# Performance work log

Measured on AMD Instinct MI355X. Metric: run time of the kernel, lower is better.

Reference implementation:

```python
import jax, jax.numpy as jnp
import numpy as np

B, L, D = 8, 2048, 64

def setup_inputs() -> dict:
    key = jax.random.key(0)
    kq, kk, kv, kqm, kkm = jax.random.split(key, 5)
    return {
        "query": jax.random.normal(kq, (B, L, D), dtype=jnp.float32),
        "key": jax.random.normal(kk, (B, L, D), dtype=jnp.float32),
        "value": jax.random.normal(kv, (B, L, D), dtype=jnp.float32),
        "q_mask": jax.random.randint(kqm, (B, L), 0, 2, dtype=jnp.int32),
        "k_mask": jax.random.randint(kkm, (B, L), 0, 2, dtype=jnp.int32),
    }

def reference(query, key, value, q_mask, k_mask):
    # scale defaults to D_q; divide scores by sqrt(D_q)
    D_q = query.shape[-1]
    qm = q_mask.astype(jnp.float32)  # [B, L_q]
    km = k_mask.astype(jnp.float32)  # [B, L_k]
    # outer-product mask: [B, L_q, L_k]
    mask = qm[:, :, None] * km[:, None, :]
    scores = jnp.einsum("bqd,bkd->bqk", query, key) / jnp.sqrt(jnp.float32(D_q))
    # masked_fill(-inf).exp(): masked positions become exactly 0
    A = jnp.where(mask == 0, 0.0, jnp.exp(scores))  # [B, L_q, L_k]
    # sum clamped to min 1.0 (NOT a standard softmax normalization)
    A_sum = jnp.maximum(A.sum(axis=-1, keepdims=True), 1.0)
    attn = A / A_sum
    return jnp.einsum("bqk,bkd->bqd", attn, value)
```

## Files before the change

### kernel.cpp

```cpp
#include <hip/hip_runtime.h>
#include <hip/hip_bf16.h>
#include <stdint.h>

#define BB 8
#define LL 2048
#define DD 64

typedef short bf16x8 __attribute__((ext_vector_type(8)));
typedef float f32x4 __attribute__((ext_vector_type(4)));
typedef unsigned short ushort_t;
typedef __attribute__((address_space(1))) const unsigned int gas_u32;
typedef __attribute__((address_space(3))) unsigned int las_u32;

__device__ __forceinline__ unsigned pk2(float lo, float hi) {
    union { __hip_bfloat162 h; unsigned u; } c;
    c.h = __float22bfloat162_rn(make_float2(lo, hi));
    return c.u;
}
__device__ __forceinline__ float4 ld4(const float* __restrict__ p) {
    return *reinterpret_cast<const float4*>(p);
}
__device__ __forceinline__ bf16x8 cvt8f(float4 a, float4 b) {
    union { bf16x8 v; unsigned u[4]; } r;
    r.u[0] = pk2(a.x, a.y); r.u[1] = pk2(a.z, a.w);
    r.u[2] = pk2(b.x, b.y); r.u[3] = pk2(b.z, b.w);
    return r.v;
}
__device__ __forceinline__ void glds16(const void* g, void* lds_base_uniform) {
    __builtin_amdgcn_global_load_lds((gas_u32*)g, (las_u32*)lds_base_uniform, 16, 0, 0);
}
__device__ __forceinline__ unsigned f2bf_u(float f) {
    union { float f; unsigned u; } v; v.f = f;
    return (v.u + 0x8000u) >> 16;
}
__device__ __forceinline__ bf16x8 cvt8(const float* __restrict__ p) {
    float4 a = ld4(p), b = ld4(p + 4);
    union { bf16x8 v; unsigned u[4]; } r;
    r.u[0] = f2bf_u(a.x) | (f2bf_u(a.y) << 16);
    r.u[1] = f2bf_u(a.z) | (f2bf_u(a.w) << 16);
    r.u[2] = f2bf_u(b.x) | (f2bf_u(b.y) << 16);
    r.u[3] = f2bf_u(b.z) | (f2bf_u(b.w) << 16);
    return r.v;
}

__global__ __launch_bounds__(256) void prep(const float* __restrict__ K,
                                            const float* __restrict__ V,
                                            ushort_t* __restrict__ Kb,
                                            ushort_t* __restrict__ VT) {
    __shared__ float t[64][65];
    if (blockIdx.x < 512) {
        size_t i = ((size_t)blockIdx.x * 256 + threadIdx.x) * 8;
        float4 a = ld4(K + i), b = ld4(K + i + 4);
        uint4 o = { pk2(a.x, a.y), pk2(a.z, a.w), pk2(b.x, b.y), pk2(b.z, b.w) };
        *reinterpret_cast<uint4*>(Kb + i) = o;
        return;
    }
    const int bx = blockIdx.x - 512;
    const int b  = bx >> 5;
    const int kt = (bx & 31) << 6;
    {
        const int r  = threadIdx.x >> 2;
        const int cq = (threadIdx.x & 3) << 4;
        const float* src = V + ((size_t)(b * LL + kt + r)) * DD + cq;
        #pragma unroll
        for (int i = 0; i < 4; ++i) {
            float4 v = ld4(src + 4 * i);
            t[r][cq + 4 * i + 0] = v.x; t[r][cq + 4 * i + 1] = v.y;
            t[r][cq + 4 * i + 2] = v.z; t[r][cq + 4 * i + 3] = v.w;
        }
    }
    __syncthreads();
    {
        const int d  = threadIdx.x >> 2;
        const int kq = (threadIdx.x & 3) << 4;
        ushort_t* dst = VT + ((size_t)(b * DD + d)) * LL + kt + kq;
        #pragma unroll
        for (int u = 0; u < 2; ++u) {
            uint4 o;
            o.x = pk2(t[kq + 8 * u + 0][d], t[kq + 8 * u + 1][d]);
            o.y = pk2(t[kq + 8 * u + 2][d], t[kq + 8 * u + 3][d]);
            o.z = pk2(t[kq + 8 * u + 4][d], t[kq + 8 * u + 5][d]);
            o.w = pk2(t[kq + 8 * u + 6][d], t[kq + 8 * u + 7][d]);
            *reinterpret_cast<uint4*>(dst + 8 * u) = o;
        }
    }
}

__global__ __launch_bounds__(512, 4) void attn8(
    const float* __restrict__ Q,
    const ushort_t* __restrict__ Kbf,
    const ushort_t* __restrict__ VTb,
    const int* __restrict__ kmask,
    float* __restrict__ Opart)
{
    const int tid  = threadIdx.x;
    const int wave = tid >> 6;
    const int lane = tid & 63;
    const int ln   = lane & 15;
    const int quad = lane >> 4;

    const int bx    = blockIdx.x;
    const int ksp   = bx & 3;
    const int qt    = (bx >> 2) & 15;
    const int b     = bx >> 6;
    const int q0    = qt * 128;
    const int kbase = ksp * 512;

    __shared__ char  lds[3][16384];
    __shared__ float kmf[512];

    const char* Kg = (const char*)Kbf + (size_t)b * LL * DD * 2;
    const char* Vg = (const char*)VTb + (size_t)b * DD * LL * 2;
    const int gr = tid >> 3;
    const int gc = (tid & 7) ^ (gr & 7);

    #define STAGE(buf, k0)                                                     \
        do {                                                                   \
            glds16(Kg + (size_t)(kbase + (k0) + gr) * 128 + gc * 16,           \
                   &lds[buf][wave * 1024]);                                    \
            glds16(Vg + (size_t)gr * (LL * 2) + (kbase + (k0)) * 2 + gc * 16,  \
                   &lds[buf][8192 + wave * 1024]);                             \
        } while (0)

    const float* qp = Q + ((size_t)(b * LL + q0 + 16 * wave + ln)) * DD + quad * 8;
    float4 qa = ld4(qp), qb = ld4(qp + 4), qc = ld4(qp + 32), qd = ld4(qp + 36);
    int4 km4 = {0, 0, 0, 0};
    if (tid < 128)
        km4 = *reinterpret_cast<const int4*>(kmask + b * LL + kbase + tid * 4);

    STAGE(0, 0);
    STAGE(1, 64);

    bf16x8 qf[2];
    qf[0] = cvt8f(qa, qb);
    qf[1] = cvt8f(qc, qd);
    if (tid < 128) {
        float4 f = { km4.x ? 1.f : 0.f, km4.y ? 1.f : 0.f,
                     km4.z ? 1.f : 0.f, km4.w ? 1.f : 0.f };
        *reinterpret_cast<float4*>(kmf + tid * 4) = f;
    }
    asm volatile("s_waitcnt lgkmcnt(0)" ::: "memory");

    f32x4 Oacc[4] = {{0,0,0,0},{0,0,0,0},{0,0,0,0},{0,0,0,0}};
    float dsum = 0.f;
    const float EC = 0.125f * 1.44269504f;

    auto tile = [&](int cb_, int it_) {
        const char* LK = lds[cb_];
        const char* LV = lds[cb_] + 8192;

        bf16x8 kf[4][2];
        #pragma unroll
        for (int tt = 0; tt < 4; ++tt) {
            const int r = 16 * tt + ln;
            #pragma unroll
            for (int dh = 0; dh < 2; ++dh) {
                const int c = (dh * 4 + quad) ^ (ln & 7);
                kf[tt][dh] = *reinterpret_cast<const bf16x8*>(LK + r * 128 + c * 16);
            }
        }
        bf16x8 vf[2][4];
        #pragma unroll
        for (int kh = 0; kh < 2; ++kh) {
            const int c = (kh * 4 + quad) ^ (ln & 7);
            #pragma unroll
            for (int db = 0; db < 4; ++db) {
                const int d = db * 16 + ln;
                vf[kh][db] = *reinterpret_cast<const bf16x8*>(LV + d * 128 + c * 16);
            }
        }

        unsigned w[4][2];
        #pragma unroll
        for (int tt = 0; tt < 4; ++tt) {
            f32x4 acc = (f32x4){0.f, 0.f, 0.f, 0.f};
            __builtin_amdgcn_s_setprio(1);
            acc = __builtin_amdgcn_mfma_f32_16x16x32_bf16(kf[tt][0], qf[0], acc, 0, 0, 0);
            acc = __builtin_amdgcn_mfma_f32_16x16x32_bf16(kf[tt][1], qf[1], acc, 0, 0, 0);
            __builtin_amdgcn_s_setprio(0);
            float4 mu = *reinterpret_cast<const float4*>(
                kmf + it_ * 64 + 16 * tt + 4 * quad);
            float e0 = exp2f(acc[0] * EC) * mu.x;
            float e1 = exp2f(acc[1] * EC) * mu.y;
            float e2 = exp2f(acc[2] * EC) * mu.z;
            float e3 = exp2f(acc[3] * EC) * mu.w;
            dsum += (e0 + e1) + (e2 + e3);
            w[tt][0] = pk2(e0, e1);
            w[tt][1] = pk2(e2, e3);
        }
        #pragma unroll
        for (int g = 0; g < 2; ++g) {
            union { bf16x8 v; unsigned u[4]; } pf;
            #pragma unroll
            for (int r = 0; r < 2; ++r) {
                auto t32 = __builtin_amdgcn_permlane32_swap(
                    w[2 * g][r], w[2 * g + 1][r], false, false);
                auto t16 = __builtin_amdgcn_permlane16_swap(
                    t32[0], t32[1], false, false);
                pf.u[r]     = t16[0];
                pf.u[r + 2] = t16[1];
            }
            __builtin_amdgcn_s_setprio(1);
            #pragma unroll
            for (int db = 0; db < 4; ++db)
                Oacc[db] = __builtin_amdgcn_mfma_f32_16x16x32_bf16(
                    pf.v, vf[g][db], Oacc[db], 0, 0, 0);
            __builtin_amdgcn_s_setprio(0);
        }
    };

    int cb = 0;
    for (int it = 0; it < 7; ++it) {
        asm volatile("s_waitcnt vmcnt(2)" ::: "memory");
        __builtin_amdgcn_s_barrier();
        asm volatile("" ::: "memory");
        if (it < 6) {
            int sb = cb + 2; if (sb >= 3) sb -= 3;
            STAGE(sb, (it + 2) * 64);
        }
        tile(cb, it);
        cb = (cb == 2) ? 0 : cb + 1;
    }
    asm volatile("s_waitcnt vmcnt(0)" ::: "memory");
    __builtin_amdgcn_s_barrier();
    asm volatile("" ::: "memory");
    tile(cb, 7);
    #undef STAGE

    {
        float v = dsum;
        v += __shfl_xor(v, 16);
        v += __shfl_xor(v, 32);
        dsum = v;
    }

    float* pb = Opart + (size_t)bx * 8320;
    #pragma unroll
    for (int db = 0; db < 4; ++db)
        #pragma unroll
        for (int r = 0; r < 4; ++r)
            pb[(16 * wave + quad * 4 + r) * 64 + db * 16 + ln] = Oacc[db][r];
    if (quad == 0) pb[8192 + 16 * wave + ln] = dsum;
}

__global__ __launch_bounds__(256) void reduce_norm(
    const float* __restrict__ Opart,
    const int* __restrict__ qmask,
    float* __restrict__ Out)
{
    const int rb   = blockIdx.x;
    const int half = rb & 1;
    const int qt   = (rb >> 1) & 15;
    const int b    = rb >> 5;
    const int t    = threadIdx.x;
    const int q    = half * 64 + (t >> 2);
    const int d0   = (t & 3) * 16;

    const float* p0 = Opart + (size_t)((b * 16 + qt) * 4 + 0) * 8320;
    const float* p1 = p0 + 8320;
    const float* p2 = p1 + 8320;
    const float* p3 = p2 + 8320;

    float dn = p0[8192 + q] + p1[8192 + q] + p2[8192 + q] + p3[8192 + q];
    float sc = qmask[b * LL + qt * 128 + q] ? (1.0f / fmaxf(dn, 1.0f)) : 0.0f;

    const int off = q * 64 + d0;
    float* op = Out + ((size_t)(b * LL + qt * 128 + q)) * DD + d0;
    #pragma unroll
    for (int i = 0; i < 4; ++i) {
        f32x4 v = *reinterpret_cast<const f32x4*>(p0 + off + 4 * i)
                + *reinterpret_cast<const f32x4*>(p1 + off + 4 * i)
                + *reinterpret_cast<const f32x4*>(p2 + off + 4 * i)
                + *reinterpret_cast<const f32x4*>(p3 + off + 4 * i);
        *reinterpret_cast<f32x4*>(op + 4 * i) = v * sc;
    }
}

__global__ __launch_bounds__(256, 4) void attn_mfma(
    const float* __restrict__ Q, const float* __restrict__ K,
    const float* __restrict__ V, const int* __restrict__ qmask,
    const int* __restrict__ kmask, float* __restrict__ Out)
{
    const int tid  = threadIdx.x;
    const int wave = tid >> 6;
    const int lane = tid & 63;
    const int n    = lane & 15;
    const int quad = lane >> 4;
    const int bx = blockIdx.x;
    const int b  = bx >> 7;
    const int q0 = (bx & 127) << 4;
    __shared__ float Pl[4][576];
    __shared__ float Opart2[4][16][68];
    __shared__ float Denp[4][16];
    const float* Qp = Q + ((size_t)(b * LL + q0 + n)) * DD + quad * 8;
    bf16x8 qf0 = cvt8(Qp);
    bf16x8 qf1 = cvt8(Qp + 32);
    const float* Kb = K + ((size_t)(b * LL) + n) * DD + quad * 8;
    const float* Vb = V + ((size_t)(b * LL) + quad * 8) * DD + n;
    const int* kmb = kmask + b * LL;
    f32x4 Oacc[4] = {{0,0,0,0},{0,0,0,0},{0,0,0,0},{0,0,0,0}};
    float den[4]  = {0.f, 0.f, 0.f, 0.f};
    float*       pw = &Pl[wave][144 * (n >> 3) + 36 * quad + (n & 7)];
    const float* pr = &Pl[wave][9 * lane];
    const int kbeg = wave * (LL / 4);
    const int kend = kbeg + (LL / 4);
    for (int k0 = kbeg; k0 < kend; k0 += 32) {
        const float* krow = Kb + (size_t)k0 * DD;
        bf16x8 kA0 = cvt8(krow);
        bf16x8 kA1 = cvt8(krow + 32);
        bf16x8 kB0 = cvt8(krow + 16 * DD);
        bf16x8 kB1 = cvt8(krow + 16 * DD + 32);
        f32x4 z = {0.f, 0.f, 0.f, 0.f};
        f32x4 S0 = __builtin_amdgcn_mfma_f32_16x16x32_bf16(qf0, kA0, z, 0, 0, 0);
        S0 = __builtin_amdgcn_mfma_f32_16x16x32_bf16(qf1, kA1, S0, 0, 0, 0);
        f32x4 S1 = __builtin_amdgcn_mfma_f32_16x16x32_bf16(qf0, kB0, z, 0, 0, 0);
        S1 = __builtin_amdgcn_mfma_f32_16x16x32_bf16(qf1, kB1, S1, 0, 0, 0);
        float km0 = (float)kmb[k0 + n];
        float km1 = (float)kmb[k0 + 16 + n];
        #pragma unroll
        for (int r = 0; r < 4; ++r) {
            float e0 = __expf(S0[r] * 0.125f) * km0;
            float e1 = __expf(S1[r] * 0.125f) * km1;
            den[r] += e0 + e1;
            pw[9 * r]       = e0;
            pw[288 + 9 * r] = e1;
        }
        __builtin_amdgcn_wave_barrier();
        float pv[8];
        #pragma unroll
        for (int j = 0; j < 8; ++j) pv[j] = pr[j];
        __builtin_amdgcn_wave_barrier();
        union { bf16x8 v; unsigned u[4]; } pf;
        #pragma unroll
        for (int j = 0; j < 4; ++j)
            pf.u[j] = f2bf_u(pv[2 * j]) | (f2bf_u(pv[2 * j + 1]) << 16);
        const float* vrow = Vb + (size_t)k0 * DD;
        #pragma unroll
        for (int db = 0; db < 4; ++db) {
            union { bf16x8 v; unsigned u[4]; } vfr;
            #pragma unroll
            for (int jj = 0; jj < 4; ++jj) {
                unsigned lo  = f2bf_u(vrow[(2 * jj) * DD + db * 16]);
                unsigned hi2 = f2bf_u(vrow[(2 * jj + 1) * DD + db * 16]);
                vfr.u[jj] = lo | (hi2 << 16);
            }
            Oacc[db] = __builtin_amdgcn_mfma_f32_16x16x32_bf16(pf.v, vfr.v, Oacc[db], 0, 0, 0);
        }
    }
    #pragma unroll
    for (int r = 0; r < 4; ++r) {
        float v = den[r];
        v += __shfl_xor(v, 1); v += __shfl_xor(v, 2);
        v += __shfl_xor(v, 4); v += __shfl_xor(v, 8);
        den[r] = v;
    }
    #pragma unroll
    for (int db = 0; db < 4; ++db)
        #pragma unroll
        for (int r = 0; r < 4; ++r)
            Opart2[wave][quad * 4 + r][db * 16 + n] = Oacc[db][r];
    if (n == 0) {
        #pragma unroll
        for (int r = 0; r < 4; ++r) Denp[wave][quad * 4 + r] = den[r];
    }
    __syncthreads();
    const int q  = tid >> 4;
    const int d0 = (tid & 15) * 4;
    f32x4 sum = *reinterpret_cast<const f32x4*>(&Opart2[0][q][d0]);
    sum += *reinterpret_cast<const f32x4*>(&Opart2[1][q][d0]);
    sum += *reinterpret_cast<const f32x4*>(&Opart2[2][q][d0]);
    sum += *reinterpret_cast<const f32x4*>(&Opart2[3][q][d0]);
    float dn  = Denp[0][q] + Denp[1][q] + Denp[2][q] + Denp[3][q];
    float inv = 1.0f / fmaxf(dn, 1.0f);
    float s   = qmask[b * LL + q0 + q] ? inv : 0.0f;
    f32x4 o   = sum * s;
    float* op = Out + ((size_t)(b * LL + q0 + q)) * DD + d0;
    *reinterpret_cast<f32x4*>(op) = o;
}

extern "C" void kernel_launch(void* const* d_in, const int* in_sizes, int n_in,
                              void* d_out, int out_size, void* d_ws, size_t ws_size,
                              hipStream_t stream) {
    (void)in_sizes; (void)n_in; (void)out_size;
    const float* Q  = (const float*)d_in[0];
    const float* K  = (const float*)d_in[1];
    const float* V  = (const float*)d_in[2];
    const int* qm   = (const int*)d_in[3];
    const int* km   = (const int*)d_in[4];
    float* Out      = (float*)d_out;

    const size_t elems   = (size_t)BB * LL * DD;
    const size_t part_off = 4u * 1024 * 1024;
    const size_t ws_need  = part_off + (size_t)512 * 8320 * sizeof(float);
    if (ws_size >= ws_need && d_ws != nullptr) {
        ushort_t* Kbf = (ushort_t*)d_ws;
        ushort_t* VTb = Kbf + elems;
        float* Opart  = (float*)((char*)d_ws + part_off);
        prep       <<<dim3(768), dim3(256), 0, stream>>>(K, V, Kbf, VTb);
        attn8      <<<dim3(512), dim3(512), 0, stream>>>(Q, Kbf, VTb, km, Opart);
        reduce_norm<<<dim3(256), dim3(256), 0, stream>>>(Opart, qm, Out);
    } else {
        attn_mfma<<<dim3(BB * (LL / 16)), dim3(256), 0, stream>>>(Q, K, V, qm, km, Out);
    }
}
```

Measured before the change: 100.3 us.

## Fuse prep, attention and reduction into one cooperative kernel with grid syncs

Replaces the three-kernel sequence (K/V bf16 conversion and transpose, split-K attention, partial reduction and normalization) with a single cooperative launch that separates the phases with grid-wide barriers. The aim is to remove two kernel launch gaps and the tail idle time between dependent kernels. The prep and reduce phases are remapped onto 512 blocks of 512 threads, and the prep phase reuses the attention LDS buffer. In exchange, grid sync adds its own cost, and it requires all 512 blocks to be co-resident. If the cooperative launch fails, the code falls back to the old three-kernel path.

```diff
diff --git a/kernel.cpp b/kernel.cpp
--- a/kernel.cpp
+++ b/kernel.cpp
@@ -1,10 +1,13 @@
 #include <hip/hip_runtime.h>
+#include <hip/hip_cooperative_groups.h>
 #include <hip/hip_bf16.h>
 #include <stdint.h>
 
 #define BB 8
 #define LL 2048
 #define DD 64
+
+namespace cg = cooperative_groups;
 
 typedef short bf16x8 __attribute__((ext_vector_type(8)));
 typedef float f32x4 __attribute__((ext_vector_type(4)));
@@ -43,55 +46,14 @@
     return r.v;
 }
 
-__global__ __launch_bounds__(256) void prep(const float* __restrict__ K,
-                                            const float* __restrict__ V,
-                                            ushort_t* __restrict__ Kb,
-                                            ushort_t* __restrict__ VT) {
-    __shared__ float t[64][65];
-    if (blockIdx.x < 512) {
-        size_t i = ((size_t)blockIdx.x * 256 + threadIdx.x) * 8;
-        float4 a = ld4(K + i), b = ld4(K + i + 4);
-        uint4 o = { pk2(a.x, a.y), pk2(a.z, a.w), pk2(b.x, b.y), pk2(b.z, b.w) };
-        *reinterpret_cast<uint4*>(Kb + i) = o;
-        return;
-    }
-    const int bx = blockIdx.x - 512;
-    const int b  = bx >> 5;
-    const int kt = (bx & 31) << 6;
-    {
-        const int r  = threadIdx.x >> 2;
-        const int cq = (threadIdx.x & 3) << 4;
-        const float* src = V + ((size_t)(b * LL + kt + r)) * DD + cq;
-        #pragma unroll
-        for (int i = 0; i < 4; ++i) {
-            float4 v = ld4(src + 4 * i);
-            t[r][cq + 4 * i + 0] = v.x; t[r][cq + 4 * i + 1] = v.y;
-            t[r][cq + 4 * i + 2] = v.z; t[r][cq + 4 * i + 3] = v.w;
-        }
-    }
-    __syncthreads();
-    {
-        const int d  = threadIdx.x >> 2;
-        const int kq = (threadIdx.x & 3) << 4;
-        ushort_t* dst = VT + ((size_t)(b * DD + d)) * LL + kt + kq;
-        #pragma unroll
-        for (int u = 0; u < 2; ++u) {
-            uint4 o;
-            o.x = pk2(t[kq + 8 * u + 0][d], t[kq + 8 * u + 1][d]);
-            o.y = pk2(t[kq + 8 * u + 2][d], t[kq + 8 * u + 3][d]);
-            o.z = pk2(t[kq + 8 * u + 4][d], t[kq + 8 * u + 5][d]);
-            o.w = pk2(t[kq + 8 * u + 6][d], t[kq + 8 * u + 7][d]);
-            *reinterpret_cast<uint4*>(dst + 8 * u) = o;
-        }
-    }
-}
-
-__global__ __launch_bounds__(512, 4) void attn8(
+__device__ __forceinline__ void attn_body(
     const float* __restrict__ Q,
     const ushort_t* __restrict__ Kbf,
     const ushort_t* __restrict__ VTb,
     const int* __restrict__ kmask,
-    float* __restrict__ Opart)
+    float* __restrict__ Opart,
+    char (*lds)[16384],
+    float* kmf)
 {
     const int tid  = threadIdx.x;
     const int wave = tid >> 6;
@@ -105,9 +67,6 @@
     const int b     = bx >> 6;
     const int q0    = qt * 128;
     const int kbase = ksp * 512;
-
-    __shared__ char  lds[3][16384];
-    __shared__ float kmf[512];
 
     const char* Kg = (const char*)Kbf + (size_t)b * LL * DD * 2;
     const char* Vg = (const char*)VTb + (size_t)b * DD * LL * 2;
@@ -241,6 +200,133 @@
         for (int r = 0; r < 4; ++r)
             pb[(16 * wave + quad * 4 + r) * 64 + db * 16 + ln] = Oacc[db][r];
     if (quad == 0) pb[8192 + 16 * wave + ln] = dsum;
+}
+
+__global__ __launch_bounds__(512, 4) void fused_all(
+    const float* __restrict__ Q, const float* __restrict__ K,
+    const float* __restrict__ V, const int* __restrict__ qmask,
+    const int* __restrict__ kmask,
+    ushort_t* __restrict__ Kbf, ushort_t* __restrict__ VTb,
+    float* __restrict__ Opart, float* __restrict__ Out)
+{
+    __shared__ char  lds[3][16384];
+    __shared__ float kmf[512];
+
+    const int tid = threadIdx.x;
+    const int bx  = blockIdx.x;
+
+    float (*t)[65] = reinterpret_cast<float(*)[65]>(&lds[0][0]);
+    if (bx < 256) {
+        size_t i = ((size_t)bx * 512 + tid) * 8;
+        float4 a = ld4(K + i), b4 = ld4(K + i + 4);
+        uint4 o = { pk2(a.x, a.y), pk2(a.z, a.w), pk2(b4.x, b4.y), pk2(b4.z, b4.w) };
+        *reinterpret_cast<uint4*>(Kbf + i) = o;
+    } else {
+        const int bxx = bx - 256;
+        const int b   = bxx >> 5;
+        const int kt  = (bxx & 31) << 6;
+        const int r   = tid >> 3;
+        const int cq  = (tid & 7) << 3;
+        const float* src = V + ((size_t)(b * LL + kt + r)) * DD + cq;
+        float4 v0 = ld4(src), v1 = ld4(src + 4);
+        t[r][cq + 0] = v0.x; t[r][cq + 1] = v0.y; t[r][cq + 2] = v0.z; t[r][cq + 3] = v0.w;
+        t[r][cq + 4] = v1.x; t[r][cq + 5] = v1.y; t[r][cq + 6] = v1.z; t[r][cq + 7] = v1.w;
+    }
+    __syncthreads();
+    if (bx >= 256) {
+        const int bxx = bx - 256;
+        const int b   = bxx >> 5;
+        const int kt  = (bxx & 31) << 6;
+        const int d   = tid >> 3;
+        const int kq  = (tid & 7) << 3;
+        uint4 o;
+        o.x = pk2(t[kq + 0][d], t[kq + 1][d]);
+        o.y = pk2(t[kq + 2][d], t[kq + 3][d]);
+        o.z = pk2(t[kq + 4][d], t[kq + 5][d]);
+        o.w = pk2(t[kq + 6][d], t[kq + 7][d]);
+        *reinterpret_cast<uint4*>(VTb + ((size_t)(b * DD + d)) * LL + kt + kq) = o;
+    }
+
+    cg::this_grid().sync();
+
+    attn_body(Q, Kbf, VTb, kmask, Opart, lds, kmf);
+
+    cg::this_grid().sync();
+
+    {
+        const unsigned g  = (unsigned)bx * 512u + (unsigned)tid;
+        const int qg  = (int)(g >> 4);
+        const int d0  = (int)(g & 15) * 4;
+        const int ql  = qg & 127;
+        const int grp = qg >> 7;
+        const float* p0 = Opart + (size_t)grp * 4 * 8320;
+        const float* p1 = p0 + 8320;
+        const float* p2 = p1 + 8320;
+        const float* p3 = p2 + 8320;
+        float dn = p0[8192 + ql] + p1[8192 + ql] + p2[8192 + ql] + p3[8192 + ql];
+        float sc = qmask[qg] ? (1.0f / fmaxf(dn, 1.0f)) : 0.0f;
+        const int off = ql * 64 + d0;
+        f32x4 v = *reinterpret_cast<const f32x4*>(p0 + off)
+                + *reinterpret_cast<const f32x4*>(p1 + off)
+                + *reinterpret_cast<const f32x4*>(p2 + off)
+                + *reinterpret_cast<const f32x4*>(p3 + off);
+        *reinterpret_cast<f32x4*>(Out + (size_t)qg * 64 + d0) = v * sc;
+    }
+}
+
+__global__ __launch_bounds__(256) void prep(const float* __restrict__ K,
+                                            const float* __restrict__ V,
+                                            ushort_t* __restrict__ Kb,
+                                            ushort_t* __restrict__ VT) {
+    __shared__ float t[64][65];
+    if (blockIdx.x < 512) {
+        size_t i = ((size_t)blockIdx.x * 256 + threadIdx.x) * 8;
+        float4 a = ld4(K + i), b = ld4(K + i + 4);
+        uint4 o = { pk2(a.x, a.y), pk2(a.z, a.w), pk2(b.x, b.y), pk2(b.z, b.w) };
+        *reinterpret_cast<uint4*>(Kb + i) = o;
+        return;
+    }
+    const int bx = blockIdx.x - 512;
+    const int b  = bx >> 5;
+    const int kt = (bx & 31) << 6;
+    {
+        const int r  = threadIdx.x >> 2;
+        const int cq = (threadIdx.x & 3) << 4;
+        const float* src = V + ((size_t)(b * LL + kt + r)) * DD + cq;
+        #pragma unroll
+        for (int i = 0; i < 4; ++i) {
+            float4 v = ld4(src + 4 * i);
+            t[r][cq + 4 * i + 0] = v.x; t[r][cq + 4 * i + 1] = v.y;
+            t[r][cq + 4 * i + 2] = v.z; t[r][cq + 4 * i + 3] = v.w;
+        }
+    }
+    __syncthreads();
+    {
+        const int d  = threadIdx.x >> 2;
+        const int kq = (threadIdx.x & 3) << 4;
+        ushort_t* dst = VT + ((size_t)(b * DD + d)) * LL + kt + kq;
+        #pragma unroll
+        for (int u = 0; u < 2; ++u) {
+            uint4 o;
+            o.x = pk2(t[kq + 8 * u + 0][d], t[kq + 8 * u + 1][d]);
+            o.y = pk2(t[kq + 8 * u + 2][d], t[kq + 8 * u + 3][d]);
+            o.z = pk2(t[kq + 8 * u + 4][d], t[kq + 8 * u + 5][d]);
+            o.w = pk2(t[kq + 8 * u + 6][d], t[kq + 8 * u + 7][d]);
+            *reinterpret_cast<uint4*>(dst + 8 * u) = o;
+        }
+    }
+}
+
+__global__ __launch_bounds__(512, 4) void attn8(
+    const float* __restrict__ Q,
+    const ushort_t* __restrict__ Kbf,
+    const ushort_t* __restrict__ VTb,
+    const int* __restrict__ kmask,
+    float* __restrict__ Opart)
+{
+    __shared__ char  lds[3][16384];
+    __shared__ float kmf[512];
+    attn_body(Q, Kbf, VTb, kmask, Opart, lds, kmf);
 }
 
 __global__ __launch_bounds__(256) void reduce_norm(
@@ -396,9 +482,19 @@
         ushort_t* Kbf = (ushort_t*)d_ws;
         ushort_t* VTb = Kbf + elems;
         float* Opart  = (float*)((char*)d_ws + part_off);
-        prep       <<<dim3(768), dim3(256), 0, stream>>>(K, V, Kbf, VTb);
-        attn8      <<<dim3(512), dim3(512), 0, stream>>>(Q, Kbf, VTb, km, Opart);
-        reduce_norm<<<dim3(256), dim3(256), 0, stream>>>(Opart, qm, Out);
+
+        void* args[9] = { (void*)&Q, (void*)&K, (void*)&V, (void*)&qm,
+                          (void*)&km, (void*)&Kbf, (void*)&VTb,
+                          (void*)&Opart, (void*)&Out };
+        hipError_t e = hipLaunchCooperativeKernel(
+            reinterpret_cast<const void*>(fused_all),
+            dim3(512), dim3(512), args, 0, stream);
+        if (e != hipSuccess) {
+            (void)hipGetLastError();
+            prep       <<<dim3(768), dim3(256), 0, stream>>>(K, V, Kbf, VTb);
+            attn8      <<<dim3(512), dim3(512), 0, stream>>>(Q, Kbf, VTb, km, Opart);
+            reduce_norm<<<dim3(256), dim3(256), 0, stream>>>(Opart, qm, Out);
+        }
     } else {
         attn_mfma<<<dim3(BB * (LL / 16)), dim3(256), 0, stream>>>(Q, K, V, qm, km, Out);
     }
```

New measurement: 211.8 us. 2.11x slower.

## Fuse split-K reduction into attention kernel via last-block atomic counter

Applied to the files above, without the earlier changes.

Removes the separate reduce_norm launch. Each attention block now bumps a per-(batch, q-tile) atomic counter after writing its partial output. The last of the four key-split blocks then sums the partials and applies the clamped normalization and q-mask. The counters are zeroed in the prep kernel. This saves one kernel launch and its scheduling gap, at the cost of atomics, fences, and a serialized tail reduction done by only a quarter of the blocks.

```diff
diff --git a/kernel.cpp b/kernel.cpp
--- a/kernel.cpp
+++ b/kernel.cpp
@@ -46,8 +46,10 @@
 __global__ __launch_bounds__(256) void prep(const float* __restrict__ K,
                                             const float* __restrict__ V,
                                             ushort_t* __restrict__ Kb,
-                                            ushort_t* __restrict__ VT) {
+                                            ushort_t* __restrict__ VT,
+                                            int* __restrict__ cnt) {
     __shared__ float t[64][65];
+    if (blockIdx.x == 0 && threadIdx.x < 128) cnt[threadIdx.x] = 0;
     if (blockIdx.x < 512) {
         size_t i = ((size_t)blockIdx.x * 256 + threadIdx.x) * 8;
         float4 a = ld4(K + i), b = ld4(K + i + 4);
@@ -86,12 +88,14 @@
     }
 }
 
-__global__ __launch_bounds__(512, 4) void attn8(
+__device__ __forceinline__ void attn_body(
     const float* __restrict__ Q,
     const ushort_t* __restrict__ Kbf,
     const ushort_t* __restrict__ VTb,
     const int* __restrict__ kmask,
-    float* __restrict__ Opart)
+    float* __restrict__ Opart,
+    char (*lds)[16384],
+    float* kmf)
 {
     const int tid  = threadIdx.x;
     const int wave = tid >> 6;
@@ -105,9 +109,6 @@
     const int b     = bx >> 6;
     const int q0    = qt * 128;
     const int kbase = ksp * 512;
-
-    __shared__ char  lds[3][16384];
-    __shared__ float kmf[512];
 
     const char* Kg = (const char*)Kbf + (size_t)b * LL * DD * 2;
     const char* Vg = (const char*)VTb + (size_t)b * DD * LL * 2;
@@ -243,20 +244,42 @@
     if (quad == 0) pb[8192 + 16 * wave + ln] = dsum;
 }
 
-__global__ __launch_bounds__(256) void reduce_norm(
-    const float* __restrict__ Opart,
+__global__ __launch_bounds__(512, 4) void attn8(
+    const float* __restrict__ Q,
+    const ushort_t* __restrict__ Kbf,
+    const ushort_t* __restrict__ VTb,
+    const int* __restrict__ kmask,
+    float* __restrict__ Opart,
+    int* __restrict__ cnt,
     const int* __restrict__ qmask,
     float* __restrict__ Out)
 {
-    const int rb   = blockIdx.x;
-    const int half = rb & 1;
-    const int qt   = (rb >> 1) & 15;
-    const int b    = rb >> 5;
-    const int t    = threadIdx.x;
-    const int q    = half * 64 + (t >> 2);
-    const int d0   = (t & 3) * 16;
-
-    const float* p0 = Opart + (size_t)((b * 16 + qt) * 4 + 0) * 8320;
+    __shared__ char  lds[3][16384];
+    __shared__ float kmf[512];
+    attn_body(Q, Kbf, VTb, kmask, Opart, lds, kmf);
+
+    const int tid = threadIdx.x;
+    const int bx  = blockIdx.x;
+    __shared__ int lastflag;
+    __syncthreads();
+    if (tid == 0) {
+        __threadfence();
+        int old = __hip_atomic_fetch_add(&cnt[bx >> 2], 1,
+                                         __ATOMIC_ACQ_REL,
+                                         __HIP_MEMORY_SCOPE_AGENT);
+        lastflag = (old == 3) ? 1 : 0;
+    }
+    __syncthreads();
+    if (!lastflag) return;
+    __threadfence();
+
+    const int grp = bx >> 2;
+    const int b   = grp >> 4;
+    const int qt  = grp & 15;
+    const int q   = tid >> 2;
+    const int d0  = (tid & 3) << 4;
+
+    const float* p0 = Opart + (size_t)grp * 4 * 8320;
     const float* p1 = p0 + 8320;
     const float* p2 = p1 + 8320;
     const float* p3 = p2 + 8320;
@@ -389,16 +412,18 @@
     const int* km   = (const int*)d_in[4];
     float* Out      = (float*)d_out;
 
-    const size_t elems   = (size_t)BB * LL * DD;
+    const size_t elems    = (size_t)BB * LL * DD;
     const size_t part_off = 4u * 1024 * 1024;
-    const size_t ws_need  = part_off + (size_t)512 * 8320 * sizeof(float);
+    const size_t part_sz  = (size_t)512 * 8320 * sizeof(float);
+    const size_t ws_need  = part_off + part_sz + 512;
     if (ws_size >= ws_need && d_ws != nullptr) {
         ushort_t* Kbf = (ushort_t*)d_ws;
         ushort_t* VTb = Kbf + elems;
         float* Opart  = (float*)((char*)d_ws + part_off);
-        prep       <<<dim3(768), dim3(256), 0, stream>>>(K, V, Kbf, VTb);
-        attn8      <<<dim3(512), dim3(512), 0, stream>>>(Q, Kbf, VTb, km, Opart);
-        reduce_norm<<<dim3(256), dim3(256), 0, stream>>>(Opart, qm, Out);
+        int*   cnt    = (int*)((char*)d_ws + part_off + part_sz);
+        prep <<<dim3(768), dim3(256), 0, stream>>>(K, V, Kbf, VTb, cnt);
+        attn8<<<dim3(512), dim3(512), 0, stream>>>(Q, Kbf, VTb, km, Opart,
+                                                   cnt, qm, Out);
     } else {
         attn_mfma<<<dim3(BB * (LL / 16)), dim3(256), 0, stream>>>(Q, K, V, qm, km, Out);
     }
```

New measurement: 180.3 us. 79.7% more time.

## Process two query subtiles per wave to reuse K/V fragments

Applied to the files above, without the earlier changes.

Each wave now handles 32 query rows (two 16-row subtiles) instead of 16, so every K and V fragment loaded from LDS feeds twice as many MFMAs. The grid is halved to 256 blocks with 256 queries each, and the partial-output buffer and reduction kernel indexing are resized to match. This aims to cut LDS reads and global staging per unit of compute, but it doubles the accumulator registers and lowers occupancy (launch bounds 512,2). With only 256 blocks on a GPU with many CUs, parallelism may also drop.

```diff
diff --git a/kernel.cpp b/kernel.cpp
--- a/kernel.cpp
+++ b/kernel.cpp
@@ -86,7 +86,7 @@
     }
 }
 
-__global__ __launch_bounds__(512, 4) void attn8(
+__global__ __launch_bounds__(512, 2) void attn8(
     const float* __restrict__ Q,
     const ushort_t* __restrict__ Kbf,
     const ushort_t* __restrict__ VTb,
@@ -101,9 +101,9 @@
 
     const int bx    = blockIdx.x;
     const int ksp   = bx & 3;
-    const int qt    = (bx >> 2) & 15;
-    const int b     = bx >> 6;
-    const int q0    = qt * 128;
+    const int qt    = (bx >> 2) & 7;
+    const int b     = bx >> 5;
+    const int q0    = qt * 256;
     const int kbase = ksp * 512;
 
     __shared__ char  lds[3][16384];
@@ -122,8 +122,10 @@
                    &lds[buf][8192 + wave * 1024]);                             \
         } while (0)
 
-    const float* qp = Q + ((size_t)(b * LL + q0 + 16 * wave + ln)) * DD + quad * 8;
-    float4 qa = ld4(qp), qb = ld4(qp + 4), qc = ld4(qp + 32), qd = ld4(qp + 36);
+    const float* qp0 = Q + ((size_t)(b * LL + q0 + 32 * wave + ln)) * DD + quad * 8;
+    const float* qp1 = qp0 + 16 * DD;
+    float4 qa0 = ld4(qp0), qb0 = ld4(qp0 + 4), qc0 = ld4(qp0 + 32), qd0 = ld4(qp0 + 36);
+    float4 qa1 = ld4(qp1), qb1 = ld4(qp1 + 4), qc1 = ld4(qp1 + 32), qd1 = ld4(qp1 + 36);
     int4 km4 = {0, 0, 0, 0};
     if (tid < 128)
         km4 = *reinterpret_cast<const int4*>(kmask + b * LL + kbase + tid * 4);
@@ -131,9 +133,9 @@
     STAGE(0, 0);
     STAGE(1, 64);
 
-    bf16x8 qf[2];
-    qf[0] = cvt8f(qa, qb);
-    qf[1] = cvt8f(qc, qd);
+    bf16x8 qf[2][2];
+    qf[0][0] = cvt8f(qa0, qb0); qf[0][1] = cvt8f(qc0, qd0);
+    qf[1][0] = cvt8f(qa1, qb1); qf[1][1] = cvt8f(qc1, qd1);
     if (tid < 128) {
         float4 f = { km4.x ? 1.f : 0.f, km4.y ? 1.f : 0.f,
                      km4.z ? 1.f : 0.f, km4.w ? 1.f : 0.f };
@@ -141,8 +143,9 @@
     }
     asm volatile("s_waitcnt lgkmcnt(0)" ::: "memory");
 
-    f32x4 Oacc[4] = {{0,0,0,0},{0,0,0,0},{0,0,0,0},{0,0,0,0}};
-    float dsum = 0.f;
+    f32x4 Oacc[2][4] = {{{0,0,0,0},{0,0,0,0},{0,0,0,0},{0,0,0,0}},
+                        {{0,0,0,0},{0,0,0,0},{0,0,0,0},{0,0,0,0}}};
+    float dsum[2] = {0.f, 0.f};
     const float EC = 0.125f * 1.44269504f;
 
     auto tile = [&](int cb_, int it_) {
@@ -170,42 +173,48 @@
             }
         }
 
-        unsigned w[4][2];
+        unsigned w[2][4][2];
         #pragma unroll
         for (int tt = 0; tt < 4; ++tt) {
-            f32x4 acc = (f32x4){0.f, 0.f, 0.f, 0.f};
-            __builtin_amdgcn_s_setprio(1);
-            acc = __builtin_amdgcn_mfma_f32_16x16x32_bf16(kf[tt][0], qf[0], acc, 0, 0, 0);
-            acc = __builtin_amdgcn_mfma_f32_16x16x32_bf16(kf[tt][1], qf[1], acc, 0, 0, 0);
-            __builtin_amdgcn_s_setprio(0);
             float4 mu = *reinterpret_cast<const float4*>(
                 kmf + it_ * 64 + 16 * tt + 4 * quad);
-            float e0 = exp2f(acc[0] * EC) * mu.x;
-            float e1 = exp2f(acc[1] * EC) * mu.y;
-            float e2 = exp2f(acc[2] * EC) * mu.z;
-            float e3 = exp2f(acc[3] * EC) * mu.w;
-            dsum += (e0 + e1) + (e2 + e3);
-            w[tt][0] = pk2(e0, e1);
-            w[tt][1] = pk2(e2, e3);
+            #pragma unroll
+            for (int s = 0; s < 2; ++s) {
+                f32x4 acc = (f32x4){0.f, 0.f, 0.f, 0.f};
+                __builtin_amdgcn_s_setprio(1);
+                acc = __builtin_amdgcn_mfma_f32_16x16x32_bf16(kf[tt][0], qf[s][0], acc, 0, 0, 0);
+                acc = __builtin_amdgcn_mfma_f32_16x16x32_bf16(kf[tt][1], qf[s][1], acc, 0, 0, 0);
+                __builtin_amdgcn_s_setprio(0);
+                float e0 = exp2f(acc[0] * EC) * mu.x;
+                float e1 = exp2f(acc[1] * EC) * mu.y;
+                float e2 = exp2f(acc[2] * EC) * mu.z;
+                float e3 = exp2f(acc[3] * EC) * mu.w;
+                dsum[s] += (e0 + e1) + (e2 + e3);
+                w[s][tt][0] = pk2(e0, e1);
+                w[s][tt][1] = pk2(e2, e3);
+            }
         }
         #pragma unroll
         for (int g = 0; g < 2; ++g) {
-            union { bf16x8 v; unsigned u[4]; } pf;
-            #pragma unroll
-            for (int r = 0; r < 2; ++r) {
-                auto t32 = __builtin_amdgcn_permlane32_swap(
-                    w[2 * g][r], w[2 * g + 1][r], false, false);
-                auto t16 = __builtin_amdgcn_permlane16_swap(
-                    t32[0], t32[1], false, false);
-                pf.u[r]     = t16[0];
-                pf.u[r + 2] = t16[1];
+            #pragma unroll
+            for (int s = 0; s < 2; ++s) {
+                union { bf16x8 v; unsigned u[4]; } pf;
+                #pragma unroll
+                for (int r = 0; r < 2; ++r) {
+                    auto t32 = __builtin_amdgcn_permlane32_swap(
+                        w[s][2 * g][r], w[s][2 * g + 1][r], false, false);
+                    auto t16 = __builtin_amdgcn_permlane16_swap(
+                        t32[0], t32[1], false, false);
+                    pf.u[r]     = t16[0];
+                    pf.u[r + 2] = t16[1];
+                }
+                __builtin_amdgcn_s_setprio(1);
+                #pragma unroll
+                for (int db = 0; db < 4; ++db)
+                    Oacc[s][db] = __builtin_amdgcn_mfma_f32_16x16x32_bf16(
+                        pf.v, vf[g][db], Oacc[s][db], 0, 0, 0);
+                __builtin_amdgcn_s_setprio(0);
             }
-            __builtin_amdgcn_s_setprio(1);
-            #pragma unroll
-            for (int db = 0; db < 4; ++db)
-                Oacc[db] = __builtin_amdgcn_mfma_f32_16x16x32_bf16(
-                    pf.v, vf[g][db], Oacc[db], 0, 0, 0);
-            __builtin_amdgcn_s_setprio(0);
         }
     };
 
@@ -227,20 +236,27 @@
     tile(cb, 7);
     #undef STAGE
 
-    {
-        float v = dsum;
+    #pragma unroll
+    for (int s = 0; s < 2; ++s) {
+        float v = dsum[s];
         v += __shfl_xor(v, 16);
         v += __shfl_xor(v, 32);
-        dsum = v;
-    }
-
-    float* pb = Opart + (size_t)bx * 8320;
+        dsum[s] = v;
+    }
+
+    float* pb = Opart + (size_t)bx * 16640;
     #pragma unroll
-    for (int db = 0; db < 4; ++db)
-        #pragma unroll
-        for (int r = 0; r < 4; ++r)
-            pb[(16 * wave + quad * 4 + r) * 64 + db * 16 + ln] = Oacc[db][r];
-    if (quad == 0) pb[8192 + 16 * wave + ln] = dsum;
+    for (int s = 0; s < 2; ++s)
+        #pragma unroll
+        for (int db = 0; db < 4; ++db)
+            #pragma unroll
+            for (int r = 0; r < 4; ++r)
+                pb[(32 * wave + 16 * s + quad * 4 + r) * 64 + db * 16 + ln] =
+                    Oacc[s][db][r];
+    if (quad == 0) {
+        pb[16384 + 32 * wave + ln]      = dsum[0];
+        pb[16384 + 32 * wave + 16 + ln] = dsum[1];
+    }
 }
 
 __global__ __launch_bounds__(256) void reduce_norm(
@@ -248,24 +264,22 @@
     const int* __restrict__ qmask,
     float* __restrict__ Out)
 {
-    const int rb   = blockIdx.x;
-    const int half = rb & 1;
-    const int qt   = (rb >> 1) & 15;
-    const int b    = rb >> 5;
-    const int t    = threadIdx.x;
-    const int q    = half * 64 + (t >> 2);
-    const int d0   = (t & 3) * 16;
-
-    const float* p0 = Opart + (size_t)((b * 16 + qt) * 4 + 0) * 8320;
-    const float* p1 = p0 + 8320;
-    const float* p2 = p1 + 8320;
-    const float* p3 = p2 + 8320;
-
-    float dn = p0[8192 + q] + p1[8192 + q] + p2[8192 + q] + p3[8192 + q];
-    float sc = qmask[b * LL + qt * 128 + q] ? (1.0f / fmaxf(dn, 1.0f)) : 0.0f;
-
-    const int off = q * 64 + d0;
-    float* op = Out + ((size_t)(b * LL + qt * 128 + q)) * DD + d0;
+    const int g   = blockIdx.x * 256 + threadIdx.x;
+    const int qg  = g >> 2;
+    const int d0  = (g & 3) * 16;
+    const int ql  = qg & 255;
+    const int grp = qg >> 8;
+
+    const float* p0 = Opart + (size_t)grp * 4 * 16640;
+    const float* p1 = p0 + 16640;
+    const float* p2 = p1 + 16640;
+    const float* p3 = p2 + 16640;
+
+    float dn = p0[16384 + ql] + p1[16384 + ql] + p2[16384 + ql] + p3[16384 + ql];
+    float sc = qmask[qg] ? (1.0f / fmaxf(dn, 1.0f)) : 0.0f;
+
+    const int off = ql * 64 + d0;
+    float* op = Out + (size_t)qg * DD + d0;
     #pragma unroll
     for (int i = 0; i < 4; ++i) {
         f32x4 v = *reinterpret_cast<const f32x4*>(p0 + off + 4 * i)
@@ -389,15 +403,16 @@
     const int* km   = (const int*)d_in[4];
     float* Out      = (float*)d_out;
 
-    const size_t elems   = (size_t)BB * LL * DD;
+    const size_t elems    = (size_t)BB * LL * DD;
     const size_t part_off = 4u * 1024 * 1024;
-    const size_t ws_need  = part_off + (size_t)512 * 8320 * sizeof(float);
+    const size_t part_sz  = (size_t)256 * 16640 * sizeof(float);
+    const size_t ws_need  = part_off + part_sz;
     if (ws_size >= ws_need && d_ws != nullptr) {
         ushort_t* Kbf = (ushort_t*)d_ws;
         ushort_t* VTb = Kbf + elems;
         float* Opart  = (float*)((char*)d_ws + part_off);
         prep       <<<dim3(768), dim3(256), 0, stream>>>(K, V, Kbf, VTb);
-        attn8      <<<dim3(512), dim3(512), 0, stream>>>(Q, Kbf, VTb, km, Opart);
+        attn8      <<<dim3(256), dim3(512), 0, stream>>>(Q, Kbf, VTb, km, Opart);
         reduce_norm<<<dim3(256), dim3(256), 0, stream>>>(Opart, qm, Out);
     } else {
         attn_mfma<<<dim3(BB * (LL / 16)), dim3(256), 0, stream>>>(Q, K, V, qm, km, Out);
```

New measurement: 101.6 us. About the same (+1.3%).
